# Kernel optimization log

Measured on AMD Instinct MI355X. Metric: run time of the kernel, lower is better.

Reference implementation:

```python
import jax, jax.numpy as jnp
import numpy as np

B, T, C = 4, 1024, 1024
NH, L, DHR, FF = 16, 512, 64, 4096
DK = C // NH  # 64
EPS = 1e-6
NEG = -9e15


def rms_norm(x, w):
    var = jnp.mean(jnp.square(x), axis=-1, keepdims=True)
    return x * jax.lax.rsqrt(var + EPS) * w


def rope_apply(x):
    # Faithful to RoPE module: freq = t+1, pos pairs repeated, theta = exp(-2*pos/C*ln(1e4))
    b, t, c = x.shape
    xf = x.astype(jnp.float32)
    freq = jnp.arange(t, dtype=jnp.float32)[:, None] + 1.0           # [t,1]
    pos = jnp.arange(c // 2, dtype=jnp.float32)[:, None]
    pos = jnp.repeat(pos, 2, axis=-1).reshape(1, -1)                 # [1,c] -> p0,p0,p1,p1,...
    theta = jnp.exp(-2.0 * pos / c * jnp.log(10000.0))
    cos = jnp.cos(freq * theta)                                      # [t,c]
    sin = jnp.sin(freq * theta)
    x2 = xf.reshape(b, t, c // 2, 2)
    rot = jnp.stack([-x2[..., 1], x2[..., 0]], axis=-1).reshape(b, t, c)
    return (xf * cos + rot * sin).astype(x.dtype)


def setup_inputs() -> dict:
    key = jax.random.key(0)
    ks = jax.random.split(key, 12)
    s = 0.02
    return {
        "x": jax.random.normal(ks[0], (B, T, C), jnp.float32),
        "rms1": jnp.ones((C,), jnp.float32),
        "rms2": jnp.ones((C,), jnp.float32),
        "W_dkv": s * jax.random.normal(ks[1], (C, 2 * L), jnp.float32),
        "b_dkv": jnp.zeros((2 * L,), jnp.float32),
        "W_kr": s * jax.random.normal(ks[2], (2 * L, DHR), jnp.float32),
        "b_kr": jnp.zeros((DHR,), jnp.float32),
        "W_qr": s * jax.random.normal(ks[3], (2 * L, DHR * NH), jnp.float32),
        "b_qr": jnp.zeros((DHR * NH,), jnp.float32),
        "W_kv": s * jax.random.normal(ks[4], (L, 2 * C), jnp.float32),
        "b_kv": jnp.zeros((2 * C,), jnp.float32),
        "W_q": s * jax.random.normal(ks[5], (L, C), jnp.float32),
        "b_q": jnp.zeros((C,), jnp.float32),
        "W_o": s * jax.random.normal(ks[6], (C, C), jnp.float32),
        "b_o": jnp.zeros((C,), jnp.float32),
        "W_f1": s * jax.random.normal(ks[7], (C, FF), jnp.float32),
        "b_f1": jnp.zeros((FF,), jnp.float32),
        "W_f2": s * jax.random.normal(ks[8], (FF, C), jnp.float32),
        "b_f2": jnp.zeros((C,), jnp.float32),
    }


def mla(x, W_dkv, b_dkv, W_kr, b_kr, W_qr, b_qr, W_kv, b_kv, W_q, b_q, W_o, b_o):
    b, t, c = x.shape
    comp = jnp.einsum('btc,cd->btd', x, W_dkv) + b_dkv               # [B,T,2L]
    cKV, cq = jnp.split(comp, 2, axis=-1)                            # [B,T,L] each
    # RoPE branches (computed from the compressed representation, as in source)
    kR = rope_apply(jnp.einsum('btl,ld->btd', comp, W_kr) + b_kr)    # [B,T,DHR]
    qR = rope_apply(jnp.einsum('btl,ld->btd', comp, W_qr) + b_qr)    # roped over full NH*DHR dim
    qR = qR.reshape(b, t, NH, DHR).transpose(0, 2, 1, 3)             # [B,NH,T,DHR]
    kv = jnp.einsum('btl,ld->btd', cKV, W_kv) + b_kv
    k, v = jnp.split(kv, 2, axis=-1)                                 # [B,T,C] each
    q = jnp.einsum('btl,ld->btd', cq, W_q) + b_q                     # [B,T,C]
    to_heads = lambda z: z.reshape(b, t, NH, DK).transpose(0, 2, 1, 3)
    q, k, v = to_heads(q), to_heads(k), to_heads(v)                  # [B,NH,T,DK]
    q = jnp.concatenate([q, qR], axis=-1)                            # [B,NH,T,DK+DHR]
    k = jnp.concatenate([k, jnp.broadcast_to(kR[:, None], (b, NH, t, DHR))], axis=-1)
    # manual masked softmax in fp32, scale uses DK (not DK+DHR), faithful to source
    scale = 1.0 / np.sqrt(DK)
    w = jnp.einsum('bnqd,bnkd->bnqk', q.astype(jnp.float32), k.astype(jnp.float32)) * scale
    mask = jnp.tril(jnp.ones((t, t), jnp.float32))
    w = jnp.where(mask == 0, NEG, w)
    p = jax.nn.softmax(w, axis=-1)
    o = jnp.einsum('bnqk,bnkd->bnqd', p, v.astype(jnp.float32)).astype(x.dtype)
    o = o.transpose(0, 2, 1, 3).reshape(b, t, c)
    return jnp.einsum('btc,cd->btd', o, W_o) + b_o


def ffn(x, W_f1, b_f1, W_f2, b_f2):
    h = jax.nn.gelu(jnp.einsum('btc,cf->btf', x, W_f1) + b_f1)
    return jnp.einsum('btf,fc->btc', h, W_f2) + b_f2


def reference(x, rms1, rms2, W_dkv, b_dkv, W_kr, b_kr, W_qr, b_qr,
              W_kv, b_kv, W_q, b_q, W_o, b_o, W_f1, b_f1, W_f2, b_f2):
    h = x + mla(rms_norm(x, rms1), W_dkv, b_dkv, W_kr, b_kr, W_qr, b_qr,
                W_kv, b_kv, W_q, b_q, W_o, b_o)
    out = h + ffn(rms_norm(h, rms2), W_f1, b_f1, W_f2, b_f2)
    return out
```

## Files before the change

### kernel.cpp

```cpp
#include <hip/hip_runtime.h>

typedef unsigned int u32;
typedef unsigned short u16;
typedef __bf16 bf16x8 __attribute__((ext_vector_type(8)));
typedef float f32x4 __attribute__((ext_vector_type(4)));

#define B_ 4
#define T_ 1024
#define C_ 1024
#define NH_ 16
#define L_ 512
#define DHR_ 64
#define FF_ 4096

typedef __attribute__((address_space(3))) u32 as3_u32;
typedef __attribute__((address_space(1))) u32 as1_u32;

__device__ __forceinline__ void gld16(const u16* g, u16* l) {
  __builtin_amdgcn_global_load_lds((const as1_u32*)g, (as3_u32*)l, 16, 0, 0);
}

__device__ __forceinline__ float bf2f(u16 u) {
  union { u32 i; float f; } v; v.i = ((u32)u) << 16; return v.f;
}
__device__ __forceinline__ u16 f2bf(float f) {
  union { float f; u32 i; } v; v.f = f;
  u32 r = (v.i + 0x7FFFu + ((v.i >> 16) & 1u)) >> 16;
  return (u16)r;
}

struct TransArgs {
  const float* src[8];
  u16* dst[8];
  int R[8], C[8];
  int base[9];
  const float* x;
  const float* rmsw;
  u16* xn;
};

__global__ void pre_all(TransArgs ta) {
  const int bid = blockIdx.x;
  if (bid >= ta.base[8]) {
    const int row = bid - ta.base[8];
    const int tid = threadIdx.y * 32 + threadIdx.x;
    const float* xp = ta.x + (size_t)row * C_;
    float v[4];
#pragma unroll
    for (int i = 0; i < 4; i++) v[i] = xp[tid + 256 * i];
    float ss = v[0] * v[0] + v[1] * v[1] + v[2] * v[2] + v[3] * v[3];
#pragma unroll
    for (int o = 32; o > 0; o >>= 1) ss += __shfl_down(ss, o, 64);
    __shared__ float red[4];
    if ((tid & 63) == 0) red[tid >> 6] = ss;
    __syncthreads();
    ss = red[0] + red[1] + red[2] + red[3];
    float scale = rsqrtf(ss * (1.0f / 1024.0f) + 1e-6f);
    u16* op = ta.xn + (size_t)row * C_;
#pragma unroll
    for (int i = 0; i < 4; i++)
      op[tid + 256 * i] = f2bf(v[i] * scale * ta.rmsw[tid + 256 * i]);
    return;
  }
  __shared__ float tile[32][33];
  int w = 0;
#pragma unroll
  for (int i = 1; i < 8; i++) w += (bid >= ta.base[i]);
  const int local = bid - ta.base[w];
  const int R = ta.R[w], C = ta.C[w];
  const int ctiles = C >> 5;
  const int bx = (local % ctiles) * 32;
  const int by = (local / ctiles) * 32;
  const float* in = ta.src[w];
  u16* outp = ta.dst[w];
  const int tx = threadIdx.x, ty = threadIdx.y;
  for (int i = ty; i < 32; i += 8)
    tile[i][tx] = in[(size_t)(by + i) * C + bx + tx];
  __syncthreads();
  for (int i = ty; i < 32; i += 8)
    outp[(size_t)(bx + i) * R + by + tx] = f2bf(tile[tx][i]);
}

__global__ __launch_bounds__(256) void rmsnorm_kernel(const float* __restrict__ xin,
                                                      const float* __restrict__ w,
                                                      u16* __restrict__ outp) {
  const int row = blockIdx.x;
  const int tid = threadIdx.x;
  const float* xp = xin + (size_t)row * C_;
  float v[4];
#pragma unroll
  for (int i = 0; i < 4; i++) v[i] = xp[tid + 256 * i];
  float ss = v[0] * v[0] + v[1] * v[1] + v[2] * v[2] + v[3] * v[3];
#pragma unroll
  for (int o = 32; o > 0; o >>= 1) ss += __shfl_down(ss, o, 64);
  __shared__ float red[4];
  if ((tid & 63) == 0) red[tid >> 6] = ss;
  __syncthreads();
  ss = red[0] + red[1] + red[2] + red[3];
  float scale = rsqrtf(ss * (1.0f / 1024.0f) + 1e-6f);
  u16* op = outp + (size_t)row * C_;
#pragma unroll
  for (int i = 0; i < 4; i++)
    op[tid + 256 * i] = f2bf(v[i] * scale * w[tid + 256 * i]);
}

template<int EPI, bool NCLIP, int NT>
__device__ __forceinline__ void g_body(
    u16* As, u16* Bs,
    const u16* __restrict__ A, int lda, int aoff,
    const u16* __restrict__ BT, const float* __restrict__ bias,
    const float* __restrict__ resid, void* __restrict__ out,
    int N, int Kfull, int Klen, int m0, int n0, int koff) {
  const int tid = threadIdx.x;
  const int wave = tid >> 6, lane = tid & 63;
  const int wm = wave >> 1, wn = wave & 1;
  const int quad = lane >> 4, l15 = lane & 15;
  const int srow = tid >> 3;
  const int gseg = (tid & 7) ^ (srow & 7);

  const u16* aP = A + (size_t)(m0 + srow) * lda + aoff + koff + gseg * 8;
  const u16* bP = BT + (size_t)(n0 + srow) * Kfull + koff + gseg * 8;
  u16* aL = As + tid * 8;
  u16* bL = Bs + tid * 8;
  const size_t aStep = (size_t)32 * lda;
  const size_t bStep = (size_t)32 * Kfull;

  f32x4 acc[4][NT] = {};

  for (int k0 = 0; k0 < Klen; k0 += 64) {
#pragma unroll
    for (int c = 0; c < 4; c++)
      gld16(aP + k0 + c * aStep, aL + c * 32 * 64);
#pragma unroll
    for (int c = 0; c < NT; c++)
      gld16(bP + k0 + c * bStep, bL + c * 32 * 64);
    __syncthreads();
#pragma unroll
    for (int kh = 0; kh < 2; kh++) {
      bf16x8 af[4], bfr[NT];
#pragma unroll
      for (int mt = 0; mt < 4; mt++) {
        const int r = wm * 64 + mt * 16 + l15;
        const int p = (kh * 4 + quad) ^ (r & 7);
        af[mt] = *(const bf16x8*)&As[r * 64 + p * 8];
      }
#pragma unroll
      for (int nt = 0; nt < NT; nt++) {
        const int r = wn * (NT * 16) + nt * 16 + l15;
        const int p = (kh * 4 + quad) ^ (r & 7);
        bfr[nt] = *(const bf16x8*)&Bs[r * 64 + p * 8];
      }
#pragma unroll
      for (int mt = 0; mt < 4; mt++)
#pragma unroll
        for (int nt = 0; nt < NT; nt++)
          acc[mt][nt] = __builtin_amdgcn_mfma_f32_16x16x32_bf16(af[mt], bfr[nt], acc[mt][nt], 0, 0, 0);
    }
    __syncthreads();
  }

  float bvv[NT];
#pragma unroll
  for (int nt = 0; nt < NT; nt++) {
    const int gn = n0 + wn * (NT * 16) + nt * 16 + l15;
    bvv[nt] = (EPI == 4) ? 0.0f : ((NCLIP && gn >= N) ? 0.0f : bias[gn]);
  }
#pragma unroll
  for (int mt = 0; mt < 4; mt++) {
#pragma unroll
    for (int i = 0; i < 4; i++) {
      const int gm = m0 + wm * 64 + mt * 16 + quad * 4 + i;
      const size_t rowb = (size_t)gm * N;
#pragma unroll
      for (int nt = 0; nt < NT; nt++) {
        const int gn = n0 + wn * (NT * 16) + nt * 16 + l15;
        if (NCLIP && gn >= N) continue;
        const size_t oidx = rowb + gn;
        float v = acc[mt][nt][i] + bvv[nt];
        if (EPI == 2) {
          float y = 0.7978845608028654f * (v + 0.044715f * v * v * v);
          float t = __expf(fminf(2.0f * y, 80.0f));
          v = v * t / (t + 1.0f);
        }
        if (EPI == 3) v += resid[oidx];
        if (EPI == 1 || EPI == 3 || EPI == 4) ((float*)out)[oidx] = v;
        else ((u16*)out)[oidx] = f2bf(v);
      }
    }
  }
}

template<int EPI, int NT>
__global__ __launch_bounds__(256) void gemmN(
    const u16* __restrict__ A, int lda, int aoff,
    const u16* __restrict__ BT, const float* __restrict__ bias,
    const float* __restrict__ resid, void* __restrict__ out,
    int N, int K) {
  __shared__ __align__(16) u16 As[128 * 64];
  __shared__ __align__(16) u16 Bs[NT * 32 * 64];
  g_body<EPI, false, NT>(As, Bs, A, lda, aoff, BT, bias, resid, out,
                         N, K, K, blockIdx.x * 128, blockIdx.y * (NT * 32), 0);
}

__global__ __launch_bounds__(256) void gemm128_splitk(
    const u16* __restrict__ A, int lda, const u16* __restrict__ BT,
    float* __restrict__ part, int N, int Kfull, int Klen) {
  __shared__ __align__(16) u16 As[128 * 64];
  __shared__ __align__(16) u16 Bs[128 * 64];
  const int z = blockIdx.z;
  g_body<4, false, 4>(As, Bs, A, lda, 0, BT, nullptr, nullptr,
                      part + (size_t)z * 4096 * N,
                      N, Kfull, Klen, blockIdx.x * 128, blockIdx.y * 128, z * Klen);
}

__global__ __launch_bounds__(256) void f2_reduce(
    const float* __restrict__ part, const float* __restrict__ h,
    const float* __restrict__ bias, float* __restrict__ out) {
  const size_t base = (size_t)blockIdx.x * 1024;
  const size_t PS = (size_t)4096 * 1024;
#pragma unroll
  for (int i = 0; i < 4; i++) {
    const int col = threadIdx.x + 256 * i;
    out[base + col] = h[base + col] + bias[col] + part[base + col] +
                      part[PS + base + col];
  }
}

__global__ __launch_bounds__(256) void proj_fused(
    const u16* __restrict__ comp,
    const u16* __restrict__ WT_qr, const float* __restrict__ b_qr, float* __restrict__ qr_pre,
    const u16* __restrict__ WT_kr, const float* __restrict__ b_kr, float* __restrict__ kr_pre,
    const u16* __restrict__ WT_kv, const float* __restrict__ b_kv, u16* __restrict__ kvbuf,
    const u16* __restrict__ WT_q, const float* __restrict__ b_q, u16* __restrict__ qbuf) {
  __shared__ __align__(16) u16 As[128 * 64];
  __shared__ __align__(16) u16 Bs[128 * 64];
  const int m0 = blockIdx.x * 128;
  const int ny = blockIdx.y;
  if (ny < 8)
    g_body<1, false, 4>(As, Bs, comp, 1024, 0, WT_qr, b_qr, nullptr, qr_pre, 1024, 1024, 1024, m0, ny * 128, 0);
  else if (ny == 8)
    g_body<1, true, 4>(As, Bs, comp, 1024, 0, WT_kr, b_kr, nullptr, kr_pre, 64, 1024, 1024, m0, 0, 0);
  else if (ny < 25)
    g_body<0, false, 4>(As, Bs, comp, 1024, 0, WT_kv, b_kv, nullptr, kvbuf, 2048, 512, 512, m0, (ny - 9) * 128, 0);
  else
    g_body<0, false, 4>(As, Bs, comp, 1024, 512, WT_q, b_q, nullptr, qbuf, 1024, 512, 512, m0, (ny - 25) * 128, 0);
}

__global__ __launch_bounds__(256) void rope_vtrans(
    const u16* __restrict__ qb, const float* __restrict__ qr_pre,
    const u16* __restrict__ kvb, const float* __restrict__ kr_pre,
    u16* __restrict__ Qf, u16* __restrict__ kRf, u16* __restrict__ Vf) {
  __shared__ u16 tile[64][72];
  if (blockIdx.x >= 4096) {
    const int bid2 = blockIdx.x - 4096;
    const int bh = bid2 & 63, t0 = (bid2 >> 6) * 64;
    const int b = bh >> 4, h = bh & 15;
    const int r = threadIdx.x >> 2, seg = (threadIdx.x & 3) * 16;
    const u16* src = &kvb[((size_t)(b * 1024) + t0 + r) * 2048 + 1024 + h * 64 + seg];
    *(uint4*)&tile[r][seg] = *(const uint4*)src;
    *(uint4*)&tile[r][seg + 8] = *(const uint4*)(src + 8);
    __syncthreads();
    const int d = threadIdx.x >> 2, ts = (threadIdx.x & 3) * 16;
    u16 tmp[16];
#pragma unroll
    for (int j = 0; j < 16; j++) tmp[j] = tile[ts + j][d];
    u16* dst = &Vf[((size_t)bh * 64 + d) * 1024 + t0 + ts];
    *(uint4*)dst = *(uint4*)tmp;
    *(uint4*)(dst + 8) = *(uint4*)(tmp + 8);
    return;
  }
  const int bt = blockIdx.x;
  const int b = bt >> 10, t = bt & 1023;
  const float freq = (float)(t + 1);
  for (int idx = threadIdx.x; idx < 2048; idx += 256) {
    const int h = idx >> 7, d = idx & 127;
    const size_t dst = (((size_t)(b * 16 + h)) * T_ + t) * 128 + d;
    if (d < 64) {
      Qf[dst] = qb[(size_t)bt * C_ + h * 64 + d];
    } else {
      const int dd = d - 64;
      const int g = h * 64 + dd;
      const int p = g >> 1;
      const float theta = __expf(-(float)(2 * p) * (9.210340372f / 1024.0f));
      float s, c;
      sincosf(freq * theta, &s, &c);
      const float x0 = qr_pre[(size_t)bt * 1024 + (p << 1)];
      const float x1 = qr_pre[(size_t)bt * 1024 + (p << 1) + 1];
      Qf[dst] = f2bf((g & 1) ? (x1 * c + x0 * s) : (x0 * c - x1 * s));
      if (h == 0) {
        const int p2 = dd >> 1;
        const float theta2 = __expf(-(float)(2 * p2) * (9.210340372f / 64.0f));
        float s2, c2;
        sincosf(freq * theta2, &s2, &c2);
        const float y0 = kr_pre[(size_t)bt * 64 + (p2 << 1)];
        const float y1 = kr_pre[(size_t)bt * 64 + (p2 << 1) + 1];
        kRf[(size_t)bt * 64 + dd] = f2bf((dd & 1) ? (y1 * c2 + y0 * s2) : (y0 * c2 - y1 * s2));
      }
    }
  }
}

#define KSTR 136
#define VSTR 72

__device__ __forceinline__ void attn_tile(
    u16* Ks, u16* Vt, u16* Ps,
    const u16* __restrict__ Qf, const u16* __restrict__ kvbuf,
    const u16* __restrict__ kRf, const u16* __restrict__ Vf,
    u16* __restrict__ attn_o, int b, int h, int qt) {
  const int tid = threadIdx.x;
  const int wave = tid >> 6, lane = tid & 63;
  const int quad = lane >> 4, l15 = lane & 15;
  const int q0 = qt * 64;
  const size_t bh = (size_t)(b * 16 + h);

  bf16x8 qfrag[4];
  {
    const u16* qb = &Qf[(bh * T_ + q0 + wave * 16 + l15) * 128 + quad * 8];
#pragma unroll
    for (int kc = 0; kc < 4; kc++) qfrag[kc] = *(const bf16x8*)(qb + kc * 32);
  }

  f32x4 acc_o[4] = {};
  float m_i[4], l_i[4];
#pragma unroll
  for (int i = 0; i < 4; i++) { m_i[i] = -3.0e38f; l_i[i] = 0.0f; }

  const int kr_ = tid >> 3, kcs = (tid & 7) * 16;
  const int vd = tid >> 2, vts = (tid & 3) * 16;
  u16* Pw = Ps + wave * 16 * VSTR;

  const bool isk = kcs < 64;
  const size_t rstep = isk ? (size_t)32 * 2048 : (size_t)32 * 64;

  for (int kt = 0; kt <= qt; kt++) {
    __syncthreads();
    {
      const int t_row = kt * 64 + kr_;
      const u16* s0 = isk
          ? &kvbuf[((size_t)(b * T_) + t_row) * 2048 + h * 64 + kcs]
          : &kRf[((size_t)(b * T_) + t_row) * 64 + (kcs - 64)];
      const u16* s1 = s0 + rstep;
      *(uint4*)&Ks[kr_ * KSTR + kcs] = *(const uint4*)s0;
      *(uint4*)&Ks[kr_ * KSTR + kcs + 8] = *(const uint4*)(s0 + 8);
      *(uint4*)&Ks[(kr_ + 32) * KSTR + kcs] = *(const uint4*)s1;
      *(uint4*)&Ks[(kr_ + 32) * KSTR + kcs + 8] = *(const uint4*)(s1 + 8);
      const u16* vs = &Vf[(bh * 64 + vd) * 1024 + kt * 64 + vts];
      *(uint4*)&Vt[vd * VSTR + vts] = *(const uint4*)vs;
      *(uint4*)&Vt[vd * VSTR + vts + 8] = *(const uint4*)(vs + 8);
    }
    __syncthreads();

    f32x4 acc_s[4] = {};
#pragma unroll
    for (int kc = 0; kc < 4; kc++) {
#pragma unroll
      for (int ng = 0; ng < 4; ng++) {
        bf16x8 bb = *(const bf16x8*)&Ks[(ng * 16 + l15) * KSTR + kc * 32 + quad * 8];
        acc_s[ng] = __builtin_amdgcn_mfma_f32_16x16x32_bf16(qfrag[kc], bb, acc_s[ng], 0, 0, 0);
      }
    }

    float sv[4][4];
#pragma unroll
    for (int ng = 0; ng < 4; ng++)
#pragma unroll
      for (int i = 0; i < 4; i++) {
        float s = acc_s[ng][i] * 0.125f;
        if (kt == qt && (ng * 16 + l15) > (wave * 16 + quad * 4 + i)) s = -3.0e38f;
        sv[ng][i] = s;
      }

    float alpha[4], mx[4];
#pragma unroll
    for (int i = 0; i < 4; i++) {
      float m = fmaxf(fmaxf(sv[0][i], sv[1][i]), fmaxf(sv[2][i], sv[3][i]));
#pragma unroll
      for (int off = 1; off < 16; off <<= 1) m = fmaxf(m, __shfl_xor(m, off, 64));
      float mn = fmaxf(m_i[i], m);
      alpha[i] = __expf(m_i[i] - mn);
      m_i[i] = mn;
      mx[i] = mn;
    }
    float rs[4] = {0.f, 0.f, 0.f, 0.f};
#pragma unroll
    for (int ng = 0; ng < 4; ng++)
#pragma unroll
      for (int i = 0; i < 4; i++) {
        float p = __expf(sv[ng][i] - mx[i]);
        rs[i] += p;
        Pw[(quad * 4 + i) * VSTR + ng * 16 + l15] = f2bf(p);
      }
#pragma unroll
    for (int i = 0; i < 4; i++) {
      float r = rs[i];
#pragma unroll
      for (int off = 1; off < 16; off <<= 1) r += __shfl_xor(r, off, 64);
      l_i[i] = l_i[i] * alpha[i] + r;
    }

#pragma unroll
    for (int ng = 0; ng < 4; ng++)
#pragma unroll
      for (int i = 0; i < 4; i++) acc_o[ng][i] *= alpha[i];
#pragma unroll
    for (int kc = 0; kc < 2; kc++) {
      bf16x8 a = *(const bf16x8*)&Pw[l15 * VSTR + kc * 32 + quad * 8];
#pragma unroll
      for (int ng = 0; ng < 4; ng++) {
        bf16x8 bb = *(const bf16x8*)&Vt[(ng * 16 + l15) * VSTR + kc * 32 + quad * 8];
        acc_o[ng] = __builtin_amdgcn_mfma_f32_16x16x32_bf16(a, bb, acc_o[ng], 0, 0, 0);
      }
    }
  }

  float linv[4];
#pragma unroll
  for (int i = 0; i < 4; i++) linv[i] = 1.0f / l_i[i];
#pragma unroll
  for (int ng = 0; ng < 4; ng++)
#pragma unroll
    for (int i = 0; i < 4; i++) {
      const int qrow = q0 + wave * 16 + quad * 4 + i;
      attn_o[((size_t)(b * T_) + qrow) * C_ + h * 64 + ng * 16 + l15] =
          f2bf(acc_o[ng][i] * linv[i]);
    }
}

__global__ __launch_bounds__(256) void attn_mfma(
    const u16* __restrict__ Qf, const u16* __restrict__ kvbuf,
    const u16* __restrict__ kRf, const u16* __restrict__ Vf,
    u16* __restrict__ attn_o) {
  __shared__ __align__(16) u16 Ks[64 * KSTR];
  __shared__ __align__(16) u16 Vt[64 * VSTR];
  __shared__ __align__(16) u16 Ps[4 * 16 * VSTR];
  const int bh_lin = blockIdx.x & 63;
  const int j = blockIdx.x >> 6;
  const int h = bh_lin & 15;
  const int b = bh_lin >> 4;
  attn_tile(Ks, Vt, Ps, Qf, kvbuf, kRf, Vf, attn_o, b, h, 15 - j);
  attn_tile(Ks, Vt, Ps, Qf, kvbuf, kRf, Vf, attn_o, b, h, j);
}

extern "C" void kernel_launch(void* const* d_in, const int* in_sizes, int n_in,
                              void* d_out, int out_size, void* d_ws, size_t ws_size,
                              hipStream_t stream) {
  const float* x = (const float*)d_in[0];
  const float* rms1 = (const float*)d_in[1];
  const float* rms2 = (const float*)d_in[2];
  const float* W_dkv = (const float*)d_in[3];
  const float* b_dkv = (const float*)d_in[4];
  const float* W_kr = (const float*)d_in[5];
  const float* b_kr = (const float*)d_in[6];
  const float* W_qr = (const float*)d_in[7];
  const float* b_qr = (const float*)d_in[8];
  const float* W_kv = (const float*)d_in[9];
  const float* b_kv = (const float*)d_in[10];
  const float* W_q = (const float*)d_in[11];
  const float* b_q = (const float*)d_in[12];
  const float* W_o = (const float*)d_in[13];
  const float* b_o = (const float*)d_in[14];
  const float* W_f1 = (const float*)d_in[15];
  const float* b_f1 = (const float*)d_in[16];
  const float* W_f2 = (const float*)d_in[17];
  const float* b_f2 = (const float*)d_in[18];
  float* out = (float*)d_out;

  char* ws = (char*)d_ws;
  size_t off = 0;
  auto alloc = [&](size_t bytes) -> void* {
    void* p = ws + off;
    off += (bytes + 255) & ~(size_t)255;
    return p;
  };
  u16* WT_dkv = (u16*)alloc((size_t)1024 * 1024 * 2);
  u16* WT_kr  = (u16*)alloc((size_t)128 * 1024 * 2);
  u16* WT_qr  = (u16*)alloc((size_t)1024 * 1024 * 2);
  u16* WT_kv  = (u16*)alloc((size_t)2048 * 512 * 2);
  u16* WT_q   = (u16*)alloc((size_t)1024 * 512 * 2);
  u16* WT_o   = (u16*)alloc((size_t)1024 * 1024 * 2);
  u16* WT_f1  = (u16*)alloc((size_t)4096 * 1024 * 2);
  u16* WT_f2  = (u16*)alloc((size_t)1024 * 4096 * 2);
  u16* xn1    = (u16*)alloc((size_t)4096 * 1024 * 2);
  u16* comp   = (u16*)alloc((size_t)4096 * 1024 * 2);
  float* kr_pre = (float*)alloc((size_t)4096 * 64 * 4);
  float* qr_pre = (float*)alloc((size_t)4096 * 1024 * 4);
  u16* kvbuf  = (u16*)alloc((size_t)4096 * 2048 * 2);
  u16* qbuf   = (u16*)alloc((size_t)4096 * 1024 * 2);
  u16* Qf     = (u16*)alloc((size_t)64 * 1024 * 128 * 2);
  u16* kRf    = (u16*)alloc((size_t)4096 * 64 * 2);
  u16* Vf     = (u16*)alloc((size_t)64 * 64 * 1024 * 2);
  u16* attn_o = (u16*)alloc((size_t)4096 * 1024 * 2);
  float* hbuf = (float*)alloc((size_t)4096 * 1024 * 4);
  u16* hn     = (u16*)alloc((size_t)4096 * 1024 * 2);
  u16* hid    = (u16*)alloc((size_t)4096 * 4096 * 2);
  float* partial = (float*)Qf;

  TransArgs ta;
  const float* srcs[8] = {W_dkv, W_kr, W_qr, W_kv, W_q, W_o, W_f1, W_f2};
  u16* dsts[8] = {WT_dkv, WT_kr, WT_qr, WT_kv, WT_q, WT_o, WT_f1, WT_f2};
  const int Rs[8] = {1024, 1024, 1024, 512, 512, 1024, 1024, 4096};
  const int Cs[8] = {1024, 64, 1024, 2048, 1024, 1024, 4096, 1024};
  int acc_t = 0;
  for (int i = 0; i < 8; i++) {
    ta.src[i] = srcs[i]; ta.dst[i] = dsts[i]; ta.R[i] = Rs[i]; ta.C[i] = Cs[i];
    ta.base[i] = acc_t;
    acc_t += (Rs[i] >> 5) * (Cs[i] >> 5);
  }
  ta.base[8] = acc_t;
  ta.x = x; ta.rmsw = rms1; ta.xn = xn1;
  pre_all<<<acc_t + 4096, dim3(32, 8), 0, stream>>>(ta);

  gemmN<0, 2><<<dim3(32, 16), 256, 0, stream>>>(xn1, 1024, 0, WT_dkv, b_dkv, nullptr, comp, 1024, 1024);

  proj_fused<<<dim3(32, 33), 256, 0, stream>>>(comp,
      WT_qr, b_qr, qr_pre, WT_kr, b_kr, kr_pre,
      WT_kv, b_kv, kvbuf, WT_q, b_q, qbuf);

  rope_vtrans<<<4096 + 1024, 256, 0, stream>>>(qbuf, qr_pre, kvbuf, kr_pre, Qf, kRf, Vf);

  attn_mfma<<<B_ * NH_ * 8, 256, 0, stream>>>(Qf, kvbuf, kRf, Vf, attn_o);

  gemmN<3, 2><<<dim3(32, 16), 256, 0, stream>>>(attn_o, 1024, 0, WT_o, b_o, x, hbuf, 1024, 1024);

  rmsnorm_kernel<<<4096, 256, 0, stream>>>(hbuf, rms2, hn);

  gemmN<2, 4><<<dim3(32, 32), 256, 0, stream>>>(hn, 1024, 0, WT_f1, b_f1, nullptr, hid, 4096, 1024);

  gemm128_splitk<<<dim3(32, 8, 2), 256, 0, stream>>>(hid, 4096, WT_f2, partial, 1024, 4096, 2048);
  f2_reduce<<<4096, 256, 0, stream>>>(partial, hbuf, b_f2, out);
}
```

Measured before the change: 416.5 us.

## Prefetch next K/V tile into registers and launch one q-tile per attention block

The attention kernel now gives each block a single query tile (1024 blocks, j from 0 to 15, qt = 15 - j) instead of pairing a long and a short causal tile in one 512-block launch. It also loads the next K/V tile from global memory into registers while the current tile's MFMAs and softmax run, then writes it to LDS at the next iteration. Launch bounds ask for 4 blocks per CU. The aim is more parallelism and hiding global-load latency, at the cost of uneven per-block work and extra register pressure.

```diff
diff --git a/kernel.cpp b/kernel.cpp
--- a/kernel.cpp
+++ b/kernel.cpp
@@ -303,143 +303,144 @@
 #define KSTR 136
 #define VSTR 72
 
-__device__ __forceinline__ void attn_tile(
-    u16* Ks, u16* Vt, u16* Ps,
-    const u16* __restrict__ Qf, const u16* __restrict__ kvbuf,
-    const u16* __restrict__ kRf, const u16* __restrict__ Vf,
-    u16* __restrict__ attn_o, int b, int h, int qt) {
-  const int tid = threadIdx.x;
-  const int wave = tid >> 6, lane = tid & 63;
-  const int quad = lane >> 4, l15 = lane & 15;
-  const int q0 = qt * 64;
-  const size_t bh = (size_t)(b * 16 + h);
-
-  bf16x8 qfrag[4];
-  {
-    const u16* qb = &Qf[(bh * T_ + q0 + wave * 16 + l15) * 128 + quad * 8];
-#pragma unroll
-    for (int kc = 0; kc < 4; kc++) qfrag[kc] = *(const bf16x8*)(qb + kc * 32);
-  }
-
-  f32x4 acc_o[4] = {};
-  float m_i[4], l_i[4];
-#pragma unroll
-  for (int i = 0; i < 4; i++) { m_i[i] = -3.0e38f; l_i[i] = 0.0f; }
-
-  const int kr_ = tid >> 3, kcs = (tid & 7) * 16;
-  const int vd = tid >> 2, vts = (tid & 3) * 16;
-  u16* Pw = Ps + wave * 16 * VSTR;
-
-  const bool isk = kcs < 64;
-  const size_t rstep = isk ? (size_t)32 * 2048 : (size_t)32 * 64;
-
-  for (int kt = 0; kt <= qt; kt++) {
-    __syncthreads();
-    {
-      const int t_row = kt * 64 + kr_;
-      const u16* s0 = isk
-          ? &kvbuf[((size_t)(b * T_) + t_row) * 2048 + h * 64 + kcs]
-          : &kRf[((size_t)(b * T_) + t_row) * 64 + (kcs - 64)];
-      const u16* s1 = s0 + rstep;
-      *(uint4*)&Ks[kr_ * KSTR + kcs] = *(const uint4*)s0;
-      *(uint4*)&Ks[kr_ * KSTR + kcs + 8] = *(const uint4*)(s0 + 8);
-      *(uint4*)&Ks[(kr_ + 32) * KSTR + kcs] = *(const uint4*)s1;
-      *(uint4*)&Ks[(kr_ + 32) * KSTR + kcs + 8] = *(const uint4*)(s1 + 8);
-      const u16* vs = &Vf[(bh * 64 + vd) * 1024 + kt * 64 + vts];
-      *(uint4*)&Vt[vd * VSTR + vts] = *(const uint4*)vs;
-      *(uint4*)&Vt[vd * VSTR + vts + 8] = *(const uint4*)(vs + 8);
-    }
-    __syncthreads();
-
-    f32x4 acc_s[4] = {};
-#pragma unroll
-    for (int kc = 0; kc < 4; kc++) {
-#pragma unroll
-      for (int ng = 0; ng < 4; ng++) {
-        bf16x8 bb = *(const bf16x8*)&Ks[(ng * 16 + l15) * KSTR + kc * 32 + quad * 8];
-        acc_s[ng] = __builtin_amdgcn_mfma_f32_16x16x32_bf16(qfrag[kc], bb, acc_s[ng], 0, 0, 0);
-      }
-    }
-
-    float sv[4][4];
-#pragma unroll
-    for (int ng = 0; ng < 4; ng++)
-#pragma unroll
-      for (int i = 0; i < 4; i++) {
-        float s = acc_s[ng][i] * 0.125f;
-        if (kt == qt && (ng * 16 + l15) > (wave * 16 + quad * 4 + i)) s = -3.0e38f;
-        sv[ng][i] = s;
-      }
-
-    float alpha[4], mx[4];
-#pragma unroll
-    for (int i = 0; i < 4; i++) {
-      float m = fmaxf(fmaxf(sv[0][i], sv[1][i]), fmaxf(sv[2][i], sv[3][i]));
-#pragma unroll
-      for (int off = 1; off < 16; off <<= 1) m = fmaxf(m, __shfl_xor(m, off, 64));
-      float mn = fmaxf(m_i[i], m);
-      alpha[i] = __expf(m_i[i] - mn);
-      m_i[i] = mn;
-      mx[i] = mn;
-    }
-    float rs[4] = {0.f, 0.f, 0.f, 0.f};
-#pragma unroll
-    for (int ng = 0; ng < 4; ng++)
-#pragma unroll
-      for (int i = 0; i < 4; i++) {
-        float p = __expf(sv[ng][i] - mx[i]);
-        rs[i] += p;
-        Pw[(quad * 4 + i) * VSTR + ng * 16 + l15] = f2bf(p);
-      }
-#pragma unroll
-    for (int i = 0; i < 4; i++) {
-      float r = rs[i];
-#pragma unroll
-      for (int off = 1; off < 16; off <<= 1) r += __shfl_xor(r, off, 64);
-      l_i[i] = l_i[i] * alpha[i] + r;
-    }
-
-#pragma unroll
-    for (int ng = 0; ng < 4; ng++)
-#pragma unroll
-      for (int i = 0; i < 4; i++) acc_o[ng][i] *= alpha[i];
-#pragma unroll
-    for (int kc = 0; kc < 2; kc++) {
-      bf16x8 a = *(const bf16x8*)&Pw[l15 * VSTR + kc * 32 + quad * 8];
-#pragma unroll
-      for (int ng = 0; ng < 4; ng++) {
-        bf16x8 bb = *(const bf16x8*)&Vt[(ng * 16 + l15) * VSTR + kc * 32 + quad * 8];
-        acc_o[ng] = __builtin_amdgcn_mfma_f32_16x16x32_bf16(a, bb, acc_o[ng], 0, 0, 0);
-      }
-    }
-  }
-
-  float linv[4];
-#pragma unroll
-  for (int i = 0; i < 4; i++) linv[i] = 1.0f / l_i[i];
-#pragma unroll
-  for (int ng = 0; ng < 4; ng++)
-#pragma unroll
-    for (int i = 0; i < 4; i++) {
-      const int qrow = q0 + wave * 16 + quad * 4 + i;
-      attn_o[((size_t)(b * T_) + qrow) * C_ + h * 64 + ng * 16 + l15] =
-          f2bf(acc_o[ng][i] * linv[i]);
-    }
-}
-
-__global__ __launch_bounds__(256) void attn_mfma(
+__global__ __launch_bounds__(256, 4) void attn_mfma(
     const u16* __restrict__ Qf, const u16* __restrict__ kvbuf,
     const u16* __restrict__ kRf, const u16* __restrict__ Vf,
     u16* __restrict__ attn_o) {
   __shared__ __align__(16) u16 Ks[64 * KSTR];
   __shared__ __align__(16) u16 Vt[64 * VSTR];
   __shared__ __align__(16) u16 Ps[4 * 16 * VSTR];
+
   const int bh_lin = blockIdx.x & 63;
   const int j = blockIdx.x >> 6;
   const int h = bh_lin & 15;
   const int b = bh_lin >> 4;
-  attn_tile(Ks, Vt, Ps, Qf, kvbuf, kRf, Vf, attn_o, b, h, 15 - j);
-  attn_tile(Ks, Vt, Ps, Qf, kvbuf, kRf, Vf, attn_o, b, h, j);
+  const int qt = 15 - j;
+  const int q0 = qt * 64;
+  const size_t bh = (size_t)(b * 16 + h);
+
+  const int tid = threadIdx.x;
+  const int wave = tid >> 6, lane = tid & 63;
+  const int quad = lane >> 4, l15 = lane & 15;
+
+  bf16x8 qfrag[4];
+  {
+    const u16* qb = &Qf[(bh * T_ + q0 + wave * 16 + l15) * 128 + quad * 8];
+#pragma unroll
+    for (int kc = 0; kc < 4; kc++) qfrag[kc] = *(const bf16x8*)(qb + kc * 32);
+  }
+
+  f32x4 acc_o[4] = {};
+  float m_i[4], l_i[4];
+#pragma unroll
+  for (int i = 0; i < 4; i++) { m_i[i] = -3.0e38f; l_i[i] = 0.0f; }
+
+  const int kr_ = tid >> 3, kcs = (tid & 7) * 16;
+  const int vd = tid >> 2, vts = (tid & 3) * 16;
+  u16* Pw = Ps + wave * 16 * VSTR;
+
+  const bool isk = kcs < 64;
+  const size_t rstep = isk ? (size_t)32 * 2048 : (size_t)32 * 64;
+
+  uint4 kA0, kA1, kB0, kB1, vr0, vr1;
+  auto prefetch = [&](int kt) {
+    const int t_row = kt * 64 + kr_;
+    const u16* s0 = isk
+        ? &kvbuf[((size_t)(b * T_) + t_row) * 2048 + h * 64 + kcs]
+        : &kRf[((size_t)(b * T_) + t_row) * 64 + (kcs - 64)];
+    const u16* s1 = s0 + rstep;
+    kA0 = *(const uint4*)s0; kA1 = *(const uint4*)(s0 + 8);
+    kB0 = *(const uint4*)s1; kB1 = *(const uint4*)(s1 + 8);
+    const u16* vs = &Vf[(bh * 64 + vd) * 1024 + kt * 64 + vts];
+    vr0 = *(const uint4*)vs; vr1 = *(const uint4*)(vs + 8);
+  };
+  prefetch(0);
+
+  for (int kt = 0; kt <= qt; kt++) {
+    __syncthreads();
+    *(uint4*)&Ks[kr_ * KSTR + kcs] = kA0;
+    *(uint4*)&Ks[kr_ * KSTR + kcs + 8] = kA1;
+    *(uint4*)&Ks[(kr_ + 32) * KSTR + kcs] = kB0;
+    *(uint4*)&Ks[(kr_ + 32) * KSTR + kcs + 8] = kB1;
+    *(uint4*)&Vt[vd * VSTR + vts] = vr0;
+    *(uint4*)&Vt[vd * VSTR + vts + 8] = vr1;
+    __syncthreads();
+    if (kt < qt) prefetch(kt + 1);
+
+    f32x4 acc_s[4] = {};
+#pragma unroll
+    for (int kc = 0; kc < 4; kc++) {
+#pragma unroll
+      for (int ng = 0; ng < 4; ng++) {
+        bf16x8 bb = *(const bf16x8*)&Ks[(ng * 16 + l15) * KSTR + kc * 32 + quad * 8];
+        acc_s[ng] = __builtin_amdgcn_mfma_f32_16x16x32_bf16(qfrag[kc], bb, acc_s[ng], 0, 0, 0);
+      }
+    }
+
+    float sv[4][4];
+#pragma unroll
+    for (int ng = 0; ng < 4; ng++)
+#pragma unroll
+      for (int i = 0; i < 4; i++) {
+        float s = acc_s[ng][i] * 0.125f;
+        if (kt == qt && (ng * 16 + l15) > (wave * 16 + quad * 4 + i)) s = -3.0e38f;
+        sv[ng][i] = s;
+      }
+
+    float alpha[4], mx[4];
+#pragma unroll
+    for (int i = 0; i < 4; i++) {
+      float m = fmaxf(fmaxf(sv[0][i], sv[1][i]), fmaxf(sv[2][i], sv[3][i]));
+#pragma unroll
+      for (int off = 1; off < 16; off <<= 1) m = fmaxf(m, __shfl_xor(m, off, 64));
+      float mn = fmaxf(m_i[i], m);
+      alpha[i] = __expf(m_i[i] - mn);
+      m_i[i] = mn;
+      mx[i] = mn;
+    }
+    float rs[4] = {0.f, 0.f, 0.f, 0.f};
+#pragma unroll
+    for (int ng = 0; ng < 4; ng++)
+#pragma unroll
+      for (int i = 0; i < 4; i++) {
+        float p = __expf(sv[ng][i] - mx[i]);
+        rs[i] += p;
+        Pw[(quad * 4 + i) * VSTR + ng * 16 + l15] = f2bf(p);
+      }
+#pragma unroll
+    for (int i = 0; i < 4; i++) {
+      float r = rs[i];
+#pragma unroll
+      for (int off = 1; off < 16; off <<= 1) r += __shfl_xor(r, off, 64);
+      l_i[i] = l_i[i] * alpha[i] + r;
+    }
+
+#pragma unroll
+    for (int ng = 0; ng < 4; ng++)
+#pragma unroll
+      for (int i = 0; i < 4; i++) acc_o[ng][i] *= alpha[i];
+#pragma unroll
+    for (int kc = 0; kc < 2; kc++) {
+      bf16x8 a = *(const bf16x8*)&Pw[l15 * VSTR + kc * 32 + quad * 8];
+#pragma unroll
+      for (int ng = 0; ng < 4; ng++) {
+        bf16x8 bb = *(const bf16x8*)&Vt[(ng * 16 + l15) * VSTR + kc * 32 + quad * 8];
+        acc_o[ng] = __builtin_amdgcn_mfma_f32_16x16x32_bf16(a, bb, acc_o[ng], 0, 0, 0);
+      }
+    }
+  }
+
+  float linv[4];
+#pragma unroll
+  for (int i = 0; i < 4; i++) linv[i] = 1.0f / l_i[i];
+#pragma unroll
+  for (int ng = 0; ng < 4; ng++)
+#pragma unroll
+    for (int i = 0; i < 4; i++) {
+      const int qrow = q0 + wave * 16 + quad * 4 + i;
+      attn_o[((size_t)(b * T_) + qrow) * C_ + h * 64 + ng * 16 + l15] =
+          f2bf(acc_o[ng][i] * linv[i]);
+    }
 }
 
 extern "C" void kernel_launch(void* const* d_in, const int* in_sizes, int n_in,
@@ -519,7 +520,7 @@
 
   rope_vtrans<<<4096 + 1024, 256, 0, stream>>>(qbuf, qr_pre, kvbuf, kr_pre, Qf, kRf, Vf);
 
-  attn_mfma<<<B_ * NH_ * 8, 256, 0, stream>>>(Qf, kvbuf, kRf, Vf, attn_o);
+  attn_mfma<<<B_ * NH_ * 16, 256, 0, stream>>>(Qf, kvbuf, kRf, Vf, attn_o);
 
   gemmN<3, 2><<<dim3(32, 16), 256, 0, stream>>>(attn_o, 1024, 0, WT_o, b_o, x, hbuf, 1024, 1024);
 
```

New measurement: 406.7 us. 2.4% less time.
